# Optimization experiments

Measured on AMD Instinct MI355X. Metric: run time of the kernel, lower is better.

## Reference

```python
import jax, jax.numpy as jnp
import numpy as np

IN_F = 4096
OUT_F = 4096
B, S = 4, 2048
RMS_EPS = 1e-6
Q_EPS = 1e-5


def setup_inputs() -> dict:
    key = jax.random.key(0)
    kx, kw, kb, ks = jax.random.split(key, 4)
    x = jax.random.normal(kx, (B, S, IN_F), dtype=jnp.float32)
    # ternary BitNet weight in {-1, 0, +1}, stored as float32 for the reference
    W = (jax.random.randint(kw, (OUT_F, IN_F), 0, 3) - 1).astype(jnp.float32)
    rms_weight = jnp.ones((IN_F,), dtype=jnp.float32)
    bias = jax.random.normal(kb, (OUT_F,), dtype=jnp.float32)
    weight_scale = jax.random.uniform(ks, (1,), dtype=jnp.float32) + 0.5
    return {"x": x, "W": W, "rms_weight": rms_weight, "bias": bias,
            "weight_scale": weight_scale}


def reference(x, W, rms_weight, bias, weight_scale):
    # RMSNorm (self.rms_norm applied before quantized matmul)
    var = jnp.mean(x * x, axis=-1, keepdims=True)
    h = x * jax.lax.rsqrt(var + RMS_EPS) * rms_weight
    # BitNet act_quant: per-token absmax int8 quantization
    scale = 127.0 / jnp.clip(jnp.max(jnp.abs(h), axis=-1, keepdims=True), Q_EPS)  # [B,S,1]
    q = jnp.clip(jnp.round(h * scale), -128.0, 127.0)
    # ternary GEMV per token, then dequant
    y = jnp.einsum('bsk,ok->bso', q, W) / scale  # [B,S,OUT_F]
    y = y + bias
    y = y * weight_scale  # weight_scale_mode == 'multiply'
    return y
```

## Files before the change

### kernel.cpp

```cpp
#include <hip/hip_runtime.h>

#define IN_F 4096
#define OUT_F 4096
#define NTOK 8192
#define KDIM 4096

using i32x4 = __attribute__((ext_vector_type(4))) int;
using f32x4 = __attribute__((ext_vector_type(4))) float;

__device__ __forceinline__ void gload_lds16(const void* g, void* l) {
  __builtin_amdgcn_global_load_lds(
      (const __attribute__((address_space(1))) void*)g,
      (__attribute__((address_space(3))) void*)l, 16, 0, 0);
}

#define WAITV(n) asm volatile("s_waitcnt vmcnt(" #n ")" ::: "memory")
#define BAR() do { asm volatile("" ::: "memory"); __builtin_amdgcn_s_barrier(); \
                   asm volatile("" ::: "memory"); } while (0)

__global__ __launch_bounds__(256) void rmsq_kernel(
    const float* __restrict__ x, const float* __restrict__ rmsw,
    signed char* __restrict__ q, float* __restrict__ dscale) {
  const int tok = blockIdx.x;
  const int tid = threadIdx.x;
  const f32x4* xr = (const f32x4*)(x + (size_t)tok * IN_F);
  const f32x4* wr = (const f32x4*)rmsw;

  f32x4 v[4];
  float ss = 0.f;
#pragma unroll
  for (int c = 0; c < 4; ++c) {
    v[c] = xr[c * 256 + tid];
    ss += v[c].x * v[c].x + v[c].y * v[c].y + v[c].z * v[c].z + v[c].w * v[c].w;
  }

  __shared__ float red[4];
#pragma unroll
  for (int off = 32; off > 0; off >>= 1) ss += __shfl_down(ss, off, 64);
  const int wid = tid >> 6;
  if ((tid & 63) == 0) red[wid] = ss;
  __syncthreads();
  const float tot = red[0] + red[1] + red[2] + red[3];
  const float rinv = rsqrtf(tot * (1.0f / IN_F) + 1e-6f);

  f32x4 h[4];
  float amax = 0.f;
#pragma unroll
  for (int c = 0; c < 4; ++c) {
    f32x4 w = wr[c * 256 + tid];
    h[c].x = v[c].x * rinv * w.x;
    h[c].y = v[c].y * rinv * w.y;
    h[c].z = v[c].z * rinv * w.z;
    h[c].w = v[c].w * rinv * w.w;
    amax = fmaxf(amax, fabsf(h[c].x));
    amax = fmaxf(amax, fabsf(h[c].y));
    amax = fmaxf(amax, fabsf(h[c].z));
    amax = fmaxf(amax, fabsf(h[c].w));
  }

  __syncthreads();
#pragma unroll
  for (int off = 32; off > 0; off >>= 1)
    amax = fmaxf(amax, __shfl_down(amax, off, 64));
  if ((tid & 63) == 0) red[wid] = amax;
  __syncthreads();
  amax = fmaxf(fmaxf(red[0], red[1]), fmaxf(red[2], red[3]));
  amax = fmaxf(amax, 1e-5f);
  const float qs = 127.0f / amax;
  if (tid == 0) dscale[tok] = amax * (1.0f / 127.0f);

  uint* qo = (uint*)(q + (size_t)tok * IN_F);
#pragma unroll
  for (int c = 0; c < 4; ++c) {
    float r0 = fminf(fmaxf(rintf(h[c].x * qs), -128.f), 127.f);
    float r1 = fminf(fmaxf(rintf(h[c].y * qs), -128.f), 127.f);
    float r2 = fminf(fmaxf(rintf(h[c].z * qs), -128.f), 127.f);
    float r3 = fminf(fmaxf(rintf(h[c].w * qs), -128.f), 127.f);
    uint p = ((uint)((int)r0 & 255)) | ((uint)((int)r1 & 255) << 8) |
             ((uint)((int)r2 & 255) << 16) | ((uint)((int)r3 & 255) << 24);
    qo[c * 256 + tid] = p;
  }
}

__global__ __launch_bounds__(256) void wconv_kernel(
    const float* __restrict__ W, signed char* __restrict__ Wq) {
  const int idx = blockIdx.x * 256 + threadIdx.x;
  f32x4 w = ((const f32x4*)W)[idx];
  uint p = ((uint)((int)w.x & 255)) | ((uint)((int)w.y & 255) << 8) |
           ((uint)((int)w.z & 255) << 16) | ((uint)((int)w.w & 255) << 24);
  ((uint*)Wq)[idx] = p;
}

#define BM 128
#define BN 256
#define BK 64
#define NT (KDIM / BK)
#define ATILEB (BM * BK)
#define BTILEB (BN * BK)
#define BUFB (ATILEB + BTILEB)
#define NBUF 3

__global__ __launch_bounds__(128, 1) void gemm_kernel(
    const signed char* __restrict__ A, const signed char* __restrict__ Bw,
    const float* __restrict__ dscale, const float* __restrict__ bias,
    const float* __restrict__ wscale_p, float* __restrict__ out) {
  __shared__ __align__(16) signed char lds[NBUF * BUFB];

  const int tid = threadIdx.x;
  const int lane = tid & 63;
  const int wc = tid >> 6;

  const int bid = blockIdx.x;
  const int swz = (bid & 7) * 128 + (bid >> 3);
  const int m0 = (swz & 63) * BM;
  const int n0 = (swz >> 6) * BN;

  const signed char* agp[4];
#pragma unroll
  for (int j = 0; j < 4; ++j) {
    const int u = tid + j * 128;
    const int r = u >> 2;
    const int s = (u & 3) ^ ((r >> 1) & 3);
    agp[j] = A + (size_t)(m0 + r) * KDIM + s * 16;
  }
  const signed char* bgp[8];
#pragma unroll
  for (int j = 0; j < 8; ++j) {
    const int u = tid + j * 128;
    const int r = u >> 2;
    const int s = (u & 3) ^ ((r >> 1) & 3);
    bgp[j] = Bw + (size_t)(n0 + r) * KDIM + s * 16;
  }

#define STAGE(kt, boff)                                                    \
  do {                                                                     \
    const int k0_ = (kt) * BK;                                             \
    signed char* lb_ = &lds[(boff)];                                       \
    gload_lds16(agp[0] + k0_, lb_ + (tid + 0 * 128) * 16);                 \
    gload_lds16(agp[1] + k0_, lb_ + (tid + 1 * 128) * 16);                 \
    gload_lds16(agp[2] + k0_, lb_ + (tid + 2 * 128) * 16);                 \
    gload_lds16(agp[3] + k0_, lb_ + (tid + 3 * 128) * 16);                 \
    gload_lds16(bgp[0] + k0_, lb_ + ATILEB + (tid + 0 * 128) * 16);        \
    gload_lds16(bgp[1] + k0_, lb_ + ATILEB + (tid + 1 * 128) * 16);        \
    gload_lds16(bgp[2] + k0_, lb_ + ATILEB + (tid + 2 * 128) * 16);        \
    gload_lds16(bgp[3] + k0_, lb_ + ATILEB + (tid + 3 * 128) * 16);        \
    gload_lds16(bgp[4] + k0_, lb_ + ATILEB + (tid + 4 * 128) * 16);        \
    gload_lds16(bgp[5] + k0_, lb_ + ATILEB + (tid + 5 * 128) * 16);        \
    gload_lds16(bgp[6] + k0_, lb_ + ATILEB + (tid + 6 * 128) * 16);        \
    gload_lds16(bgp[7] + k0_, lb_ + ATILEB + (tid + 7 * 128) * 16);        \
  } while (0)

  const int fr = lane & 15;
  const int ks = lane >> 4;
  int offA[8], offB[8];
#pragma unroll
  for (int mi = 0; mi < 8; ++mi) {
    const int row = mi * 16 + fr;
    offA[mi] = (row * 4 + (ks ^ ((row >> 1) & 3))) * 16;
  }
#pragma unroll
  for (int ni = 0; ni < 8; ++ni) {
    const int row = wc * 128 + ni * 16 + fr;
    offB[ni] = ATILEB + (row * 4 + (ks ^ ((row >> 1) & 3))) * 16;
  }

  i32x4 acc[8][8];
#pragma unroll
  for (int i = 0; i < 8; ++i)
#pragma unroll
    for (int j = 0; j < 8; ++j) acc[i][j] = (i32x4){0, 0, 0, 0};

  STAGE(0, 0);
  STAGE(1, BUFB);

  int br = 0;
  int bs = 2 * BUFB;
  for (int t = 0; t < NT; ++t) {
    if (t < NT - 1) WAITV(12); else WAITV(0);
    BAR();

    const signed char* bp = &lds[br];
    i32x4 af[8], bf[8];
#pragma unroll
    for (int i = 0; i < 8; ++i) af[i] = *(const i32x4*)(bp + offA[i]);
#pragma unroll
    for (int i = 0; i < 8; ++i) bf[i] = *(const i32x4*)(bp + offB[i]);

    if (t + 2 < NT) STAGE(t + 2, bs);

    __builtin_amdgcn_s_setprio(1);
#pragma unroll
    for (int mi = 0; mi < 8; ++mi)
#pragma unroll
      for (int ni = 0; ni < 8; ++ni)
        acc[mi][ni] = __builtin_amdgcn_mfma_i32_16x16x64_i8(af[mi], bf[ni],
                                                            acc[mi][ni], 0, 0, 0);
    __builtin_amdgcn_s_setprio(0);

    br += BUFB; if (br == NBUF * BUFB) br = 0;
    bs += BUFB; if (bs == NBUF * BUFB) bs = 0;
  }

  const float wsc = wscale_p[0];
  const int rbase = (lane >> 4) * 4;
  float bv[8];
#pragma unroll
  for (int ni = 0; ni < 8; ++ni) bv[ni] = bias[n0 + wc * 128 + ni * 16 + fr];
#pragma unroll
  for (int mi = 0; mi < 8; ++mi) {
#pragma unroll
    for (int r = 0; r < 4; ++r) {
      const int m = m0 + mi * 16 + rbase + r;
      const float ds = dscale[m];
      float* orow = out + (size_t)m * OUT_F + n0 + wc * 128;
#pragma unroll
      for (int ni = 0; ni < 8; ++ni) {
        orow[ni * 16 + fr] = ((float)acc[mi][ni][r] * ds + bv[ni]) * wsc;
      }
    }
  }
#undef STAGE
}

extern "C" void kernel_launch(void* const* d_in, const int* in_sizes, int n_in,
                              void* d_out, int out_size, void* d_ws, size_t ws_size,
                              hipStream_t stream) {
  const float* x = (const float*)d_in[0];
  const float* W = (const float*)d_in[1];
  const float* rmsw = (const float*)d_in[2];
  const float* bias = (const float*)d_in[3];
  const float* wscale = (const float*)d_in[4];
  float* out = (float*)d_out;

  signed char* q = (signed char*)d_ws;
  signed char* Wq = q + (size_t)NTOK * IN_F;
  float* dscale = (float*)(Wq + (size_t)OUT_F * IN_F);

  rmsq_kernel<<<NTOK, 256, 0, stream>>>(x, rmsw, q, dscale);
  wconv_kernel<<<(OUT_F * IN_F / 4) / 256, 256, 0, stream>>>(W, Wq);
  gemm_kernel<<<(NTOK / BM) * (OUT_F / BN), 128, 0, stream>>>(q, Wq, dscale,
                                                              bias, wscale, out);
}
```

Baseline: 193.1 us.

## Shrink int8 GEMM to single-wave 64x128 tiles and drop the barrier

Each GEMM workgroup becomes one wavefront computing a 64x128 output tile, replacing two waves sharing a 128x256 tile. With a single wave the per-iteration LDS barrier and the MFMA priority bumps are removed. The block-to-tile mapping is redone so that groups of blocks share N tiles. The aim is more resident workgroups per CU and no barrier stalls. The cost is lower data reuse per wave, since there are fewer MFMAs per LDS read and more global traffic for A and B.

```diff
diff --git a/kernel.cpp b/kernel.cpp
--- a/kernel.cpp
+++ b/kernel.cpp
@@ -15,8 +15,6 @@
 }
 
 #define WAITV(n) asm volatile("s_waitcnt vmcnt(" #n ")" ::: "memory")
-#define BAR() do { asm volatile("" ::: "memory"); __builtin_amdgcn_s_barrier(); \
-                   asm volatile("" ::: "memory"); } while (0)
 
 __global__ __launch_bounds__(256) void rmsq_kernel(
     const float* __restrict__ x, const float* __restrict__ rmsw,
@@ -91,8 +89,8 @@
   ((uint*)Wq)[idx] = p;
 }
 
-#define BM 128
-#define BN 256
+#define BM 64
+#define BN 128
 #define BK 64
 #define NT (KDIM / BK)
 #define ATILEB (BM * BK)
@@ -100,75 +98,74 @@
 #define BUFB (ATILEB + BTILEB)
 #define NBUF 3
 
-__global__ __launch_bounds__(128, 1) void gemm_kernel(
+__global__ __launch_bounds__(64, 1) void gemm_kernel(
     const signed char* __restrict__ A, const signed char* __restrict__ Bw,
     const float* __restrict__ dscale, const float* __restrict__ bias,
     const float* __restrict__ wscale_p, float* __restrict__ out) {
   __shared__ __align__(16) signed char lds[NBUF * BUFB];
 
-  const int tid = threadIdx.x;
-  const int lane = tid & 63;
-  const int wc = tid >> 6;
+  const int lane = threadIdx.x;
 
   const int bid = blockIdx.x;
-  const int swz = (bid & 7) * 128 + (bid >> 3);
-  const int m0 = (swz & 63) * BM;
-  const int n0 = (swz >> 6) * BN;
+  const int x = bid & 7;
+  const int j = bid >> 3;
+  const int m0 = (j >> 2) * BM;
+  const int n0 = (x * 4 + (j & 3)) * BN;
 
   const signed char* agp[4];
 #pragma unroll
-  for (int j = 0; j < 4; ++j) {
-    const int u = tid + j * 128;
+  for (int k = 0; k < 4; ++k) {
+    const int u = lane + k * 64;
     const int r = u >> 2;
     const int s = (u & 3) ^ ((r >> 1) & 3);
-    agp[j] = A + (size_t)(m0 + r) * KDIM + s * 16;
+    agp[k] = A + (size_t)(m0 + r) * KDIM + s * 16;
   }
   const signed char* bgp[8];
 #pragma unroll
-  for (int j = 0; j < 8; ++j) {
-    const int u = tid + j * 128;
+  for (int k = 0; k < 8; ++k) {
+    const int u = lane + k * 64;
     const int r = u >> 2;
     const int s = (u & 3) ^ ((r >> 1) & 3);
-    bgp[j] = Bw + (size_t)(n0 + r) * KDIM + s * 16;
+    bgp[k] = Bw + (size_t)(n0 + r) * KDIM + s * 16;
   }
 
 #define STAGE(kt, boff)                                                    \
   do {                                                                     \
     const int k0_ = (kt) * BK;                                             \
     signed char* lb_ = &lds[(boff)];                                       \
-    gload_lds16(agp[0] + k0_, lb_ + (tid + 0 * 128) * 16);                 \
-    gload_lds16(agp[1] + k0_, lb_ + (tid + 1 * 128) * 16);                 \
-    gload_lds16(agp[2] + k0_, lb_ + (tid + 2 * 128) * 16);                 \
-    gload_lds16(agp[3] + k0_, lb_ + (tid + 3 * 128) * 16);                 \
-    gload_lds16(bgp[0] + k0_, lb_ + ATILEB + (tid + 0 * 128) * 16);        \
-    gload_lds16(bgp[1] + k0_, lb_ + ATILEB + (tid + 1 * 128) * 16);        \
-    gload_lds16(bgp[2] + k0_, lb_ + ATILEB + (tid + 2 * 128) * 16);        \
-    gload_lds16(bgp[3] + k0_, lb_ + ATILEB + (tid + 3 * 128) * 16);        \
-    gload_lds16(bgp[4] + k0_, lb_ + ATILEB + (tid + 4 * 128) * 16);        \
-    gload_lds16(bgp[5] + k0_, lb_ + ATILEB + (tid + 5 * 128) * 16);        \
-    gload_lds16(bgp[6] + k0_, lb_ + ATILEB + (tid + 6 * 128) * 16);        \
-    gload_lds16(bgp[7] + k0_, lb_ + ATILEB + (tid + 7 * 128) * 16);        \
+    gload_lds16(agp[0] + k0_, lb_ + (lane + 0 * 64) * 16);                 \
+    gload_lds16(agp[1] + k0_, lb_ + (lane + 1 * 64) * 16);                 \
+    gload_lds16(agp[2] + k0_, lb_ + (lane + 2 * 64) * 16);                 \
+    gload_lds16(agp[3] + k0_, lb_ + (lane + 3 * 64) * 16);                 \
+    gload_lds16(bgp[0] + k0_, lb_ + ATILEB + (lane + 0 * 64) * 16);        \
+    gload_lds16(bgp[1] + k0_, lb_ + ATILEB + (lane + 1 * 64) * 16);        \
+    gload_lds16(bgp[2] + k0_, lb_ + ATILEB + (lane + 2 * 64) * 16);        \
+    gload_lds16(bgp[3] + k0_, lb_ + ATILEB + (lane + 3 * 64) * 16);        \
+    gload_lds16(bgp[4] + k0_, lb_ + ATILEB + (lane + 4 * 64) * 16);        \
+    gload_lds16(bgp[5] + k0_, lb_ + ATILEB + (lane + 5 * 64) * 16);        \
+    gload_lds16(bgp[6] + k0_, lb_ + ATILEB + (lane + 6 * 64) * 16);        \
+    gload_lds16(bgp[7] + k0_, lb_ + ATILEB + (lane + 7 * 64) * 16);        \
   } while (0)
 
   const int fr = lane & 15;
   const int ks = lane >> 4;
-  int offA[8], offB[8];
-#pragma unroll
-  for (int mi = 0; mi < 8; ++mi) {
+  int offA[4], offB[8];
+#pragma unroll
+  for (int mi = 0; mi < 4; ++mi) {
     const int row = mi * 16 + fr;
     offA[mi] = (row * 4 + (ks ^ ((row >> 1) & 3))) * 16;
   }
 #pragma unroll
   for (int ni = 0; ni < 8; ++ni) {
-    const int row = wc * 128 + ni * 16 + fr;
+    const int row = ni * 16 + fr;
     offB[ni] = ATILEB + (row * 4 + (ks ^ ((row >> 1) & 3))) * 16;
   }
 
-  i32x4 acc[8][8];
-#pragma unroll
-  for (int i = 0; i < 8; ++i)
-#pragma unroll
-    for (int j = 0; j < 8; ++j) acc[i][j] = (i32x4){0, 0, 0, 0};
+  i32x4 acc[4][8];
+#pragma unroll
+  for (int i = 0; i < 4; ++i)
+#pragma unroll
+    for (int jj = 0; jj < 8; ++jj) acc[i][jj] = (i32x4){0, 0, 0, 0};
 
   STAGE(0, 0);
   STAGE(1, BUFB);
@@ -177,25 +174,22 @@
   int bs = 2 * BUFB;
   for (int t = 0; t < NT; ++t) {
     if (t < NT - 1) WAITV(12); else WAITV(0);
-    BAR();
 
     const signed char* bp = &lds[br];
-    i32x4 af[8], bf[8];
-#pragma unroll
-    for (int i = 0; i < 8; ++i) af[i] = *(const i32x4*)(bp + offA[i]);
+    i32x4 af[4], bf[8];
+#pragma unroll
+    for (int i = 0; i < 4; ++i) af[i] = *(const i32x4*)(bp + offA[i]);
 #pragma unroll
     for (int i = 0; i < 8; ++i) bf[i] = *(const i32x4*)(bp + offB[i]);
 
     if (t + 2 < NT) STAGE(t + 2, bs);
 
-    __builtin_amdgcn_s_setprio(1);
-#pragma unroll
-    for (int mi = 0; mi < 8; ++mi)
+#pragma unroll
+    for (int mi = 0; mi < 4; ++mi)
 #pragma unroll
       for (int ni = 0; ni < 8; ++ni)
         acc[mi][ni] = __builtin_amdgcn_mfma_i32_16x16x64_i8(af[mi], bf[ni],
                                                             acc[mi][ni], 0, 0, 0);
-    __builtin_amdgcn_s_setprio(0);
 
     br += BUFB; if (br == NBUF * BUFB) br = 0;
     bs += BUFB; if (bs == NBUF * BUFB) bs = 0;
@@ -205,14 +199,14 @@
   const int rbase = (lane >> 4) * 4;
   float bv[8];
 #pragma unroll
-  for (int ni = 0; ni < 8; ++ni) bv[ni] = bias[n0 + wc * 128 + ni * 16 + fr];
-#pragma unroll
-  for (int mi = 0; mi < 8; ++mi) {
+  for (int ni = 0; ni < 8; ++ni) bv[ni] = bias[n0 + ni * 16 + fr];
+#pragma unroll
+  for (int mi = 0; mi < 4; ++mi) {
 #pragma unroll
     for (int r = 0; r < 4; ++r) {
       const int m = m0 + mi * 16 + rbase + r;
       const float ds = dscale[m];
-      float* orow = out + (size_t)m * OUT_F + n0 + wc * 128;
+      float* orow = out + (size_t)m * OUT_F + n0;
 #pragma unroll
       for (int ni = 0; ni < 8; ++ni) {
         orow[ni * 16 + fr] = ((float)acc[mi][ni][r] * ds + bv[ni]) * wsc;
@@ -238,6 +232,6 @@
 
   rmsq_kernel<<<NTOK, 256, 0, stream>>>(x, rmsw, q, dscale);
   wconv_kernel<<<(OUT_F * IN_F / 4) / 256, 256, 0, stream>>>(W, Wq);
-  gemm_kernel<<<(NTOK / BM) * (OUT_F / BN), 128, 0, stream>>>(q, Wq, dscale,
-                                                              bias, wscale, out);
-}
+  gemm_kernel<<<(NTOK / BM) * (OUT_F / BN), 64, 0, stream>>>(q, Wq, dscale,
+                                                             bias, wscale, out);
+}
```

New measurement: 258.7 us. 34.0% more time.
